# Optimization experiments

Hardware: AMD Instinct MI355X
Metric: run time of the kernel (lower is better)

Reference implementation:

```python
import jax, jax.numpy as jnp
import numpy as np
from jax import lax

B, T, H, C = 64, 512, 1024, 8


def setup_inputs() -> dict:
    key = jax.random.key(0)
    ks = jax.random.split(key, 7)
    encoding = jax.random.normal(ks[0], (B, T, H), dtype=jnp.float32)
    labels = jax.random.randint(ks[1], (B, 3 * T), 0, C)
    W = jax.random.normal(ks[2], (3, C, H), dtype=jnp.float32) * 0.02
    b = jax.random.normal(ks[3], (3, C), dtype=jnp.float32) * 0.02
    start_trans = jax.random.normal(ks[4], (3, C), dtype=jnp.float32) * 0.1
    end_trans = jax.random.normal(ks[5], (3, C), dtype=jnp.float32) * 0.1
    trans = jax.random.normal(ks[6], (3, C, C), dtype=jnp.float32) * 0.1
    return {"encoding": encoding, "labels": labels, "W": W, "b": b,
            "start_trans": start_trans, "end_trans": end_trans, "trans": trans}


def crf_neg_log_lik(em, tags, start, end, trans):
    # em [B,T,C], tags [B,T] -> scalar (torchcrf reduction='sum', loss = -llh)
    bsz = em.shape[0]
    # numerator: score of gold path
    em_sc = jnp.take_along_axis(em, tags[:, :, None], axis=2)[..., 0].sum(axis=1)
    tr_sc = trans[tags[:, :-1], tags[:, 1:]].sum(axis=1)
    num = start[tags[:, 0]] + em_sc + tr_sc + end[tags[:, -1]]
    # denominator: forward algorithm (log partition)
    a0 = start[None, :] + em[:, 0]  # [B,C]

    def step(a, e_t):
        a_new = jax.nn.logsumexp(a[:, :, None] + trans[None] + e_t[:, None, :], axis=1)
        return a_new, None

    aT, _ = lax.scan(step, a0, jnp.moveaxis(em[:, 1:], 1, 0))
    logZ = jax.nn.logsumexp(aT + end[None, :], axis=1)
    return -(num - logZ).sum()


def viterbi(em, start, end, trans):
    # em [B,T,C] -> best tag path [B,T] (no mask: all sequences full length)
    v0 = start[None, :] + em[:, 0]

    def step(v, e_t):
        s = v[:, :, None] + trans[None]          # [B,C_prev,C_cur]
        bp = jnp.argmax(s, axis=1)               # [B,C]
        return jnp.max(s, axis=1) + e_t, bp

    vT, bps = lax.scan(step, v0, jnp.moveaxis(em[:, 1:], 1, 0))  # bps [T-1,B,C]
    last = jnp.argmax(vT + end[None, :], axis=1)  # [B]

    def back(tag, bp):
        prev = jnp.take_along_axis(bp, tag[:, None], axis=1)[:, 0]
        return prev, prev

    _, rev = lax.scan(back, last, bps, reverse=True)  # [T-1,B], tags for t=0..T-2
    tags = jnp.concatenate([rev, last[None]], axis=0)  # [T,B]
    return tags.T


def reference(encoding, labels, W, b, start_trans, end_trans, trans):
    # three per-task projections: logits [3,B,T,C]
    logits = jnp.einsum('bth,kch->kbtc', encoding, W) + b[:, None, None, :]
    tags = jnp.stack(jnp.split(labels, 3, axis=1))  # [3,B,T] (task/process/material)
    losses = jax.vmap(crf_neg_log_lik)(logits, tags, start_trans, end_trans, trans)
    loss = losses.sum()
    pred = jax.vmap(viterbi)(logits, start_trans, end_trans, trans)  # [3,B,T]
    return loss, logits, pred
```

## Files before the change

kernel.cpp:

```cpp
#include <hip/hip_runtime.h>

#define NB 64
#define NT 512
#define NH 1024
#define NC 8
#define NK 3
#define BT (NB*NT)
#define LOGITS_N (NK*BT*NC)

#define QP1  0xB1
#define QP2  0x4E
#define ROR4 0x124
#define ROR8 0x128
#define HM   0x141

template<int CTRL>
__device__ __forceinline__ float dppf(float x) {
  return __int_as_float(__builtin_amdgcn_update_dpp(0, __float_as_int(x), CTRL, 0xF, 0xF, true));
}
template<int CTRL>
__device__ __forceinline__ int dppi(int x) {
  return __builtin_amdgcn_update_dpp(0, x, CTRL, 0xF, 0xF, true);
}

__global__ __launch_bounds__(256) void init_kernel(const float* __restrict__ W,
                                                   const float* __restrict__ bias,
                                                   float* __restrict__ Wt,
                                                   float* __restrict__ out) {
  int i = blockIdx.x * 256 + threadIdx.x;
  if (i < LOGITS_N) {
    int k = i >> 18, c = i & 7;
    out[1 + i] = bias[k * 8 + c];
  }
  if (i < 24 * NH) {
    int h = i / 24, j = i - h * 24;
    int kk = j >> 3, cc = j & 7;
    Wt[i] = W[kk * NC * NH + cc * NH + h];
  }
  if (i == 0) out[0] = 0.0f;
}

__global__ __launch_bounds__(256, 4) void proj_kernel(const float* __restrict__ enc,
                                                      const float* __restrict__ Wt,
                                                      float* __restrict__ out) {
  __shared__ float smem[8704];
  const int tid = threadIdx.x;
  const int lane = tid & 63;
  const int q = tid >> 6;
  const int hs = blockIdx.x & 1;
  const int rb = blockIdx.x >> 1;
  const int row0 = rb * 64;
  const int hbase = hs * 512 + q * 128;
  const float* eb = enc + (size_t)row0 * 1024 + hbase;
  float* sE0 = smem + q * 2176;

  float acc[24];
#pragma unroll
  for (int j = 0; j < 24; ++j) acc[j] = 0.0f;

  float4 pfc[4], pfn[4];
  auto loadChunk = [&](int ch, float4* pf) {
#pragma unroll
    for (int s = 0; s < 4; ++s) {
      int f = lane + 64 * s;
      pf[s] = *(const float4*)(eb + (size_t)(f >> 2) * 1024 + ch * 16 + (f & 3) * 4);
    }
  };
  auto stageChunk = [&](int buf, const float4* pf) {
    float* d = sE0 + buf * 1088;
#pragma unroll
    for (int s = 0; s < 4; ++s) {
      int f = lane + 64 * s;
      float* p = d + (f >> 2) * 17 + (f & 3) * 4;
      p[0] = pf[s].x; p[1] = pf[s].y; p[2] = pf[s].z; p[3] = pf[s].w;
    }
  };

  loadChunk(0, pfc);
  stageChunk(0, pfc);
  loadChunk(1, pfc);

#pragma unroll 1
  for (int ch = 0; ch < 8; ++ch) {
    const int buf = ch & 1;
    if (ch < 6) loadChunk(ch + 2, pfn);
    const float* wrow = Wt + __builtin_amdgcn_readfirstlane((hbase + ch * 16) * 24);
    const float* er = sE0 + buf * 1088 + lane * 17;
#pragma unroll 4
    for (int h = 0; h < 16; ++h) {
      float e = er[h];
      const float* wr = wrow + h * 24;
#pragma unroll
      for (int j = 0; j < 24; ++j)
        acc[j] = fmaf(e, wr[j], acc[j]);
    }
    if (ch < 7) {
      stageChunk(buf ^ 1, pfc);
#pragma unroll
      for (int s = 0; s < 4; ++s) pfc[s] = pfn[s];
    }
  }

  __syncthreads();
  float* sp = smem + q * 1792;
#pragma unroll
  for (int j4 = 0; j4 < 24; j4 += 4)
    *(float4*)&sp[lane * 28 + j4] = make_float4(acc[j4], acc[j4+1], acc[j4+2], acc[j4+3]);
  __syncthreads();

  const int r = tid >> 2, j0 = (tid & 3) * 6;
#pragma unroll
  for (int u = 0; u < 6; ++u) {
    int j = j0 + u;
    float s = smem[0 * 1792 + r * 28 + j] + smem[1 * 1792 + r * 28 + j]
            + smem[2 * 1792 + r * 28 + j] + smem[3 * 1792 + r * 28 + j];
    atomicAdd(&out[1 + (size_t)(j >> 3) * (BT * 8) + (size_t)(row0 + r) * 8 + (j & 7)], s);
  }
}

__global__ __launch_bounds__(512) void crf_kernel(const int* __restrict__ labels,
                                                  const float* __restrict__ startT,
                                                  const float* __restrict__ endT,
                                                  const float* __restrict__ trans,
                                                  float* __restrict__ d_out) {
  __shared__ float sA[32 * 64];
  __shared__ float sVB[32 * 8];
  __shared__ int   sBP[512];
  __shared__ int   sMap[32 * 8];
  __shared__ int   sEnt[32];
  __shared__ float sRed[32];
  __shared__ unsigned char sTags[512];
  __shared__ int sTerm;

  const int tid = threadIdx.x;
  const int lane = tid & 63;
  const int w = tid >> 6;
  const int c = lane & 7;
  const int p = (lane >> 3) & 7;
  const int role = (blockIdx.x >= 192);
  const int seq = role ? blockIdx.x - 192 : blockIdx.x;
  const int k = seq >> 6, b = seq & 63;
  const float* em = d_out + 1 + ((size_t)k * BT + (size_t)b * 512) * 8;
  const float* trk = trans + k * 64;
  const int* lab = labels + b * (NK * NT) + k * NT;

  float Txc[8];
#pragma unroll
  for (int kk = 0; kk < 8; ++kk) Txc[kk] = trk[(c ^ kk) * 8 + c];
  const float Tpc = trk[p * 8 + c];
  const float startc = startT[k * 8 + c];
  const float endc = endT[k * 8 + c];

  if (!role) {
    float Mxc[8];
#pragma unroll
    for (int kk = 0; kk < 8; ++kk) Mxc[kk] = __expf(Txc[kk]);

#pragma unroll 1
    for (int it = 0; it < 4; ++it) {
      const int i = w * 4 + it;
      const int t0 = i * 16;
      const int te = (t0 + 16 < 512) ? (t0 + 16) : 511;
      float EX[16];
      EX[0] = em[(t0 + 1) * 8 + c];
#pragma unroll
      for (int j = 1; j < 16; ++j) {
        int t = t0 + 1 + j;
        EX[j] = (t <= te) ? __expf(em[t * 8 + c]) : 1.0f;
      }
      float V = __expf(Tpc + EX[0]);
#pragma unroll
      for (int j = 1; j < 16; ++j) {
        int t = t0 + 1 + j;
        if (t <= te) {
          float x1 = dppf<QP1>(V), x2 = dppf<QP2>(V), x3 = dppf<QP2>(x1);
          float x7 = dppf<HM>(V), x6 = dppf<QP1>(x7), x5 = dppf<QP2>(x7), x4 = dppf<QP2>(x6);
          float s01 = fmaf(x1, Mxc[1], V * Mxc[0]);
          float s23 = fmaf(x3, Mxc[3], x2 * Mxc[2]);
          float s45 = fmaf(x5, Mxc[5], x4 * Mxc[4]);
          float s67 = fmaf(x7, Mxc[7], x6 * Mxc[6]);
          V = ((s01 + s23) + (s45 + s67)) * EX[j];
        }
        if (j == 8) V *= 0x1p-32f;
      }
      sA[i * 64 + lane] = V;
    }
    __syncthreads();

    float logZ = 0.0f;
    if (w == 0) {
      float al = __expf(startc + em[c]);
      float lz = 0.0f;
#pragma unroll 1
      for (int i = 0; i < 32; ++i) {
        const float* Ai = &sA[i * 64];
        float A0 = Ai[(c ^ 0) * 8 + c], A1 = Ai[(c ^ 1) * 8 + c];
        float A2 = Ai[(c ^ 2) * 8 + c], A3 = Ai[(c ^ 3) * 8 + c];
        float A4 = Ai[(c ^ 4) * 8 + c], A5 = Ai[(c ^ 5) * 8 + c];
        float A6 = Ai[(c ^ 6) * 8 + c], A7 = Ai[(c ^ 7) * 8 + c];
        float a1 = dppf<QP1>(al), a2 = dppf<QP2>(al), a3 = dppf<QP2>(a1);
        float a4 = dppf<ROR4>(al), a5 = dppf<ROR4>(a1), a6 = dppf<ROR4>(a2), a7 = dppf<ROR4>(a3);
        float s01 = fmaf(a1, A1, al * A0);
        float s23 = fmaf(a3, A3, a2 * A2);
        float s45 = fmaf(a5, A5, a4 * A4);
        float s67 = fmaf(a7, A7, a6 * A6);
        float s = (s01 + s23) + (s45 + s67);
        float ss = s;
        ss += dppf<QP1>(ss); ss += dppf<QP2>(ss); ss += dppf<ROR4>(ss);
        lz += __logf(ss);
        al = s * (1.0f / ss);
      }
      float se = al * __expf(endc);
      se += dppf<QP1>(se); se += dppf<QP2>(se); se += dppf<ROR4>(se);
      logZ = lz + __logf(se) + 1024.0f * 0.69314718055994531f;
    } else {
      int idx = (w - 1) * 64 + lane;
      float ns = 0.0f;
      {
        int tg = lab[idx];
        ns += em[(size_t)idx * 8 + tg] + trk[tg * 8 + lab[idx + 1]];
      }
      if (idx < 64) {
        int t = idx + 448;
        int tg = lab[t];
        ns += em[(size_t)t * 8 + tg];
        if (t < 511) ns += trk[tg * 8 + lab[t + 1]];
      }
      ns += dppf<QP1>(ns); ns += dppf<QP2>(ns); ns += dppf<HM>(ns); ns += dppf<ROR8>(ns);
      if ((lane & 15) == 0) sRed[(w - 1) * 4 + (lane >> 4)] = ns;
    }
    __syncthreads();
    if (tid == 0) {
      float num = startT[k * 8 + lab[0]] + endT[k * 8 + lab[511]];
#pragma unroll
      for (int u = 0; u < 28; ++u) num += sRed[u];
      atomicAdd(d_out, logZ - num);
    }
  } else {
#pragma unroll 1
    for (int it = 0; it < 4; ++it) {
      const int i = w * 4 + it;
      const int t0 = i * 16;
      const int te = (t0 + 16 < 512) ? (t0 + 16) : 511;
      float emv[16];
#pragma unroll
      for (int j = 0; j < 16; ++j) {
        int t = t0 + 1 + j;
        emv[j] = (t <= te) ? em[t * 8 + c] : 0.0f;
      }
      float V = Tpc + emv[0];
#pragma unroll
      for (int j = 1; j < 16; ++j) {
        int t = t0 + 1 + j;
        if (t <= te) {
          float x1 = dppf<QP1>(V), x2 = dppf<QP2>(V), x3 = dppf<QP2>(x1);
          float x7 = dppf<HM>(V), x6 = dppf<QP1>(x7), x5 = dppf<QP2>(x7), x4 = dppf<QP2>(x6);
          float c0 = V + Txc[0], c1 = x1 + Txc[1], c2 = x2 + Txc[2], c3 = x3 + Txc[3];
          float c4 = x4 + Txc[4], c5 = x5 + Txc[5], c6 = x6 + Txc[6], c7 = x7 + Txc[7];
          float m0 = fmaxf(fmaxf(c0, c1), c2);
          float m1 = fmaxf(fmaxf(c3, c4), c5);
          float m2 = fmaxf(c6, c7);
          V = fmaxf(fmaxf(m0, m1), m2) + emv[j];
        }
      }
      sA[i * 64 + lane] = V;
    }
    __syncthreads();

    if (w == 0) {
      float v = startc + em[c];
#pragma unroll 1
      for (int i = 0; i < 32; ++i) {
        if (lane < 8) sVB[i * 8 + c] = v;
        const float* Ai = &sA[i * 64];
        float A0 = Ai[(c ^ 0) * 8 + c], A1 = Ai[(c ^ 1) * 8 + c];
        float A2 = Ai[(c ^ 2) * 8 + c], A3 = Ai[(c ^ 3) * 8 + c];
        float A4 = Ai[(c ^ 4) * 8 + c], A5 = Ai[(c ^ 5) * 8 + c];
        float A6 = Ai[(c ^ 6) * 8 + c], A7 = Ai[(c ^ 7) * 8 + c];
        float a1 = dppf<QP1>(v), a2 = dppf<QP2>(v), a3 = dppf<QP2>(a1);
        float a4 = dppf<ROR4>(v), a5 = dppf<ROR4>(a1), a6 = dppf<ROR4>(a2), a7 = dppf<ROR4>(a3);
        float c0 = v + A0, c1 = a1 + A1, c2 = a2 + A2, c3 = a3 + A3;
        float c4 = a4 + A4, c5 = a5 + A5, c6 = a6 + A6, c7 = a7 + A7;
        float m0 = fmaxf(fmaxf(c0, c1), c2);
        float m1 = fmaxf(fmaxf(c3, c4), c5);
        float m2 = fmaxf(c6, c7);
        v = fmaxf(fmaxf(m0, m1), m2);
      }
      float lv = v + endc;
      int li = c;
      {
        float ov; int oi; bool take;
        ov = dppf<QP1>(lv); oi = dppi<QP1>(li);
        take = (ov > lv) || (ov == lv && oi < li); lv = take ? ov : lv; li = take ? oi : li;
        ov = dppf<QP2>(lv); oi = dppi<QP2>(li);
        take = (ov > lv) || (ov == lv && oi < li); lv = take ? ov : lv; li = take ? oi : li;
        ov = dppf<ROR4>(lv); oi = dppi<ROR4>(li);
        take = (ov > lv) || (ov == lv && oi < li); lv = take ? ov : lv; li = take ? oi : li;
      }
      if (lane == 0) sTerm = li;
    }
    __syncthreads();

    if (w < 4) {
      const int u = lane >> 3;
      const int i = w * 8 + u;
      const int t0 = i * 16;
      const int te = (t0 + 16 < 512) ? (t0 + 16) : 511;
      float emv[16];
#pragma unroll
      for (int j = 0; j < 16; ++j) {
        int t = t0 + 1 + j;
        emv[j] = (t <= te) ? em[t * 8 + c] : 0.0f;
      }
      float v = sVB[i * 8 + c];
#pragma unroll
      for (int j = 0; j < 16; ++j) {
        int t = t0 + 1 + j;
        if (t <= te) {
          float x1 = dppf<QP1>(v), x2 = dppf<QP2>(v), x3 = dppf<QP2>(x1);
          float x7 = dppf<HM>(v), x6 = dppf<QP1>(x7), x5 = dppf<QP2>(x7), x4 = dppf<QP2>(x6);
          float c0 = v + Txc[0], c1 = x1 + Txc[1], c2 = x2 + Txc[2], c3 = x3 + Txc[3];
          float c4 = x4 + Txc[4], c5 = x5 + Txc[5], c6 = x6 + Txc[6], c7 = x7 + Txc[7];
          float m0 = fmaxf(fmaxf(c0, c1), c2);
          float m1 = fmaxf(fmaxf(c3, c4), c5);
          float m2 = fmaxf(c6, c7);
          float best = fmaxf(fmaxf(m0, m1), m2);
          int a0 = (c0 == best) ? (c ^ 0) : 8;
          int a1i = (c1 == best) ? (c ^ 1) : 8;
          int a2i = (c2 == best) ? (c ^ 2) : 8;
          int a3i = (c3 == best) ? (c ^ 3) : 8;
          int a4i = (c4 == best) ? (c ^ 4) : 8;
          int a5i = (c5 == best) ? (c ^ 5) : 8;
          int a6i = (c6 == best) ? (c ^ 6) : 8;
          int a7i = (c7 == best) ? (c ^ 7) : 8;
          int arg = min(min(min(a0, a1i), min(a2i, a3i)),
                        min(min(a4i, a5i), min(a6i, a7i)));
          v = best + emv[j];
          int wd = arg << (3 * c);
          wd |= dppi<QP1>(wd); wd |= dppi<QP2>(wd); wd |= dppi<HM>(wd);
          if ((lane & 7) == 0) sBP[t] = wd;
        }
      }
    }
    __syncthreads();

    if (w < 4) {
      const int u = lane >> 3;
      const int i = w * 8 + u;
      const int t0 = i * 16;
      const int te = (t0 + 16 < 512) ? (t0 + 16) : 511;
      int tag = c;
#pragma unroll
      for (int j = 16; j >= 1; --j) {
        int t = t0 + j;
        if (t <= te) tag = (sBP[t] >> (3 * tag)) & 7;
      }
      sMap[i * 8 + c] = tag;
    }
    __syncthreads();
    if (tid == 0) {
      int cur = sTerm;
#pragma unroll 1
      for (int i = 31; i >= 0; --i) { cur = sMap[i * 8 + cur]; sEnt[i] = cur; }
    }
    __syncthreads();
    if (w == 0 && lane < 32) {
      const int i = lane;
      const int t0 = i * 16;
      const int te = (t0 + 16 < 512) ? (t0 + 16) : 511;
      int tag = (i == 31) ? sTerm : sEnt[i + 1];
      if (i == 31) sTags[511] = (unsigned char)tag;
#pragma unroll
      for (int j = 16; j >= 1; --j) {
        int t = t0 + j;
        if (t <= te) { tag = (sBP[t] >> (3 * tag)) & 7; sTags[t - 1] = (unsigned char)tag; }
      }
    }
    __syncthreads();
    float* outp = d_out + 1 + LOGITS_N + (size_t)seq * 512;
    outp[tid] = (float)sTags[tid];
  }
}

extern "C" void kernel_launch(void* const* d_in, const int* in_sizes, int n_in,
                              void* d_out, int out_size, void* d_ws, size_t ws_size,
                              hipStream_t stream) {
  const float* enc    = (const float*)d_in[0];
  const int*   labels = (const int*)  d_in[1];
  const float* W      = (const float*)d_in[2];
  const float* bias   = (const float*)d_in[3];
  const float* startT = (const float*)d_in[4];
  const float* endT   = (const float*)d_in[5];
  const float* trans  = (const float*)d_in[6];
  float* out = (float*)d_out;
  float* Wt  = (float*)d_ws;

  init_kernel<<<dim3(3072), dim3(256), 0, stream>>>(W, bias, Wt, out);
  proj_kernel<<<dim3(1024), dim3(256), 0, stream>>>(enc, Wt, out);
  crf_kernel<<<dim3(384), dim3(512), 0, stream>>>(labels, startT, endT, trans, out);
}
```

Before: 257.9 us.

## Restructure projection to full-H row blocks with swizzled LDS and direct stores

The projection kernel now gives each block 64 full rows across the whole hidden dimension. Whole 256-column stages are staged through a larger XOR-swizzled shared buffer, with chunk order rotated per block. Because each block owns complete rows, the bias pre-fill in the init kernel and the atomicAdd accumulation are replaced by plain stores with the bias added in. This removes a pass writing the logits buffer and the atomics, at the cost of fewer blocks (512), lower occupancy (launch bounds 2) and more registers for 16 prefetched float4s.

```diff
diff --git a/kernel.cpp b/kernel.cpp
--- a/kernel.cpp
+++ b/kernel.cpp
@@ -24,14 +24,9 @@
 }
 
 __global__ __launch_bounds__(256) void init_kernel(const float* __restrict__ W,
-                                                   const float* __restrict__ bias,
                                                    float* __restrict__ Wt,
                                                    float* __restrict__ out) {
   int i = blockIdx.x * 256 + threadIdx.x;
-  if (i < LOGITS_N) {
-    int k = i >> 18, c = i & 7;
-    out[1 + i] = bias[k * 8 + c];
-  }
   if (i < 24 * NH) {
     int h = i / 24, j = i - h * 24;
     int kk = j >> 3, cc = j & 7;
@@ -40,81 +35,78 @@
   if (i == 0) out[0] = 0.0f;
 }
 
-__global__ __launch_bounds__(256, 4) void proj_kernel(const float* __restrict__ enc,
+__global__ __launch_bounds__(256, 2) void proj_kernel(const float* __restrict__ enc,
                                                       const float* __restrict__ Wt,
+                                                      const float* __restrict__ bias,
                                                       float* __restrict__ out) {
-  __shared__ float smem[8704];
+  __shared__ float smem[64 * 256];
   const int tid = threadIdx.x;
   const int lane = tid & 63;
-  const int q = tid >> 6;
-  const int hs = blockIdx.x & 1;
-  const int rb = blockIdx.x >> 1;
-  const int row0 = rb * 64;
-  const int hbase = hs * 512 + q * 128;
-  const float* eb = enc + (size_t)row0 * 1024 + hbase;
-  float* sE0 = smem + q * 2176;
+  const int w = tid >> 6;
+  const int row0 = blockIdx.x * 64;
+  const int chrot = blockIdx.x & 3;
+  const float* eb = enc + (size_t)row0 * 1024;
 
   float acc[24];
 #pragma unroll
   for (int j = 0; j < 24; ++j) acc[j] = 0.0f;
 
-  float4 pfc[4], pfn[4];
-  auto loadChunk = [&](int ch, float4* pf) {
-#pragma unroll
-    for (int s = 0; s < 4; ++s) {
-      int f = lane + 64 * s;
-      pf[s] = *(const float4*)(eb + (size_t)(f >> 2) * 1024 + ch * 16 + (f & 3) * 4);
-    }
+  float4 pf[16];
+  auto loadStage = [&](int ci) {
+    const int cx = ci ^ chrot;
+    const float* p = eb + (size_t)w * 1024 + cx * 256 + lane * 4;
+#pragma unroll
+    for (int i = 0; i < 16; ++i)
+      pf[i] = *(const float4*)(p + (size_t)i * 4096);
   };
-  auto stageChunk = [&](int buf, const float4* pf) {
-    float* d = sE0 + buf * 1088;
-#pragma unroll
-    for (int s = 0; s < 4; ++s) {
-      int f = lane + 64 * s;
-      float* p = d + (f >> 2) * 17 + (f & 3) * 4;
-      p[0] = pf[s].x; p[1] = pf[s].y; p[2] = pf[s].z; p[3] = pf[s].w;
+  auto writeStage = [&]() {
+#pragma unroll
+    for (int i = 0; i < 16; ++i) {
+      const int r = i * 4 + w;
+      const int slot = lane ^ (r & 7);
+      *(float4*)&smem[r * 256 + slot * 4] = pf[i];
     }
   };
 
-  loadChunk(0, pfc);
-  stageChunk(0, pfc);
-  loadChunk(1, pfc);
-
-#pragma unroll 1
-  for (int ch = 0; ch < 8; ++ch) {
-    const int buf = ch & 1;
-    if (ch < 6) loadChunk(ch + 2, pfn);
-    const float* wrow = Wt + __builtin_amdgcn_readfirstlane((hbase + ch * 16) * 24);
-    const float* er = sE0 + buf * 1088 + lane * 17;
+  loadStage(0);
+  writeStage();
+
+#pragma unroll 1
+  for (int ch = 0; ch < 4; ++ch) {
+    __syncthreads();
+    if (ch < 3) loadStage(ch + 1);
+    const int cx = ch ^ chrot;
+    const float* wbase = Wt + __builtin_amdgcn_readfirstlane((cx * 256 + w * 64) * 24);
 #pragma unroll 4
-    for (int h = 0; h < 16; ++h) {
-      float e = er[h];
-      const float* wr = wrow + h * 24;
-#pragma unroll
-      for (int j = 0; j < 24; ++j)
-        acc[j] = fmaf(e, wr[j], acc[j]);
-    }
-    if (ch < 7) {
-      stageChunk(buf ^ 1, pfc);
-#pragma unroll
-      for (int s = 0; s < 4; ++s) pfc[s] = pfn[s];
-    }
+    for (int hh = 0; hh < 16; ++hh) {
+      const int slot = (w * 16 + hh) ^ (lane & 7);
+      float4 e4 = *(const float4*)&smem[lane * 256 + slot * 4];
+      const float ev[4] = {e4.x, e4.y, e4.z, e4.w};
+      const float* wr = wbase + hh * 96;
+#pragma unroll
+      for (int m = 0; m < 4; ++m) {
+        const float e = ev[m];
+        const float* wm = wr + m * 24;
+#pragma unroll
+        for (int j = 0; j < 24; ++j) acc[j] = fmaf(e, wm[j], acc[j]);
+      }
+    }
+    __syncthreads();
+    if (ch < 3) writeStage();
   }
 
-  __syncthreads();
-  float* sp = smem + q * 1792;
+  float* sp = smem + w * 1792;
 #pragma unroll
   for (int j4 = 0; j4 < 24; j4 += 4)
     *(float4*)&sp[lane * 28 + j4] = make_float4(acc[j4], acc[j4+1], acc[j4+2], acc[j4+3]);
   __syncthreads();
-
   const int r = tid >> 2, j0 = (tid & 3) * 6;
 #pragma unroll
   for (int u = 0; u < 6; ++u) {
-    int j = j0 + u;
+    const int j = j0 + u;
     float s = smem[0 * 1792 + r * 28 + j] + smem[1 * 1792 + r * 28 + j]
-            + smem[2 * 1792 + r * 28 + j] + smem[3 * 1792 + r * 28 + j];
-    atomicAdd(&out[1 + (size_t)(j >> 3) * (BT * 8) + (size_t)(row0 + r) * 8 + (j & 7)], s);
+            + smem[2 * 1792 + r * 28 + j] + smem[3 * 1792 + r * 28 + j] + bias[j];
+    out[1 + (size_t)(j >> 3) * (BT * 8) + (size_t)(row0 + r) * 8 + (j & 7)] = s;
   }
 }
 
@@ -395,7 +387,7 @@
   float* out = (float*)d_out;
   float* Wt  = (float*)d_ws;
 
-  init_kernel<<<dim3(3072), dim3(256), 0, stream>>>(W, bias, Wt, out);
-  proj_kernel<<<dim3(1024), dim3(256), 0, stream>>>(enc, Wt, out);
+  init_kernel<<<dim3(96), dim3(256), 0, stream>>>(W, Wt, out);
+  proj_kernel<<<dim3(512), dim3(256), 0, stream>>>(enc, Wt, bias, out);
   crf_kernel<<<dim3(384), dim3(512), 0, stream>>>(labels, startT, endT, trans, out);
 }
```

New measurement: 272.8 us. +5.8%, slower.
